# Kernel tuning notes

Measured on AMD Instinct MI355X. Metric: run time of the kernel, lower is better.

## Reference

```python
import jax, jax.numpy as jnp
import numpy as np

N_NODES = 100000
N_EDGES = 3200000
D_IN = 256
D_OUT = 256


def setup_inputs() -> dict:
    key = jax.random.key(0)
    k1, k2, k3, k4, k5 = jax.random.split(key, 5)
    x = jax.random.normal(k1, (N_NODES, D_IN), dtype=jnp.float32)
    weight = jax.random.normal(k2, (D_IN, D_OUT), dtype=jnp.float32)
    edge_rows = jax.random.randint(k3, (N_EDGES,), 0, N_NODES, dtype=jnp.int32)
    edge_cols = jax.random.randint(k4, (N_EDGES,), 0, N_NODES, dtype=jnp.int32)
    edge_vals = jax.random.uniform(k5, (N_EDGES,), dtype=jnp.float32)
    return {"x": x, "weight": weight, "edge_rows": edge_rows,
            "edge_cols": edge_cols, "edge_vals": edge_vals}


def reference(x, weight, edge_rows, edge_cols, edge_vals):
    # GraphConvolution forward (eval mode, dense features, no bias):
    #   xw  = x @ W                      [N, D_OUT]
    #   out = relu(A_sparse @ xw)        A given as COO edge list
    xw = x @ weight  # [N, D_OUT]
    msgs = edge_vals[:, None] * xw[edge_cols]  # gather source features, scale
    agg = jax.ops.segment_sum(msgs, edge_rows, num_segments=N_NODES)
    return jax.nn.relu(agg)
```

## Files before the change

kernel.cpp:

```cpp
#include <hip/hip_runtime.h>
#include <hip/hip_bf16.h>

#define N_NODES 100000
#define N_EDGES 3200000
#define D 256

#define RSH2 8
#define RPB2 256
#define NB2 ((N_NODES + RPB2 - 1) / RPB2)
#define FILL_CH 14336
#define NBLK_F ((N_EDGES + FILL_CH - 1) / FILL_CH)
#define MAX_BREC 9216

typedef __attribute__((ext_vector_type(8))) short short8;
typedef __attribute__((ext_vector_type(4))) float floatx4;

__device__ __forceinline__ unsigned short f32_to_bf16_rne(float f) {
    unsigned int u = __float_as_uint(f);
    u += 0x7FFFu + ((u >> 16) & 1u);
    return (unsigned short)(u >> 16);
}
__device__ __forceinline__ float bf16_bits_to_f32(unsigned short b) {
    return __uint_as_float(((unsigned int)b) << 16);
}
__device__ __forceinline__ float blo(unsigned int x) { return __uint_as_float(x << 16); }
__device__ __forceinline__ float bhi(unsigned int x) { return __uint_as_float(x & 0xFFFF0000u); }

__global__ __launch_bounds__(256) void convert_w_k(const float* __restrict__ w,
                                                   unsigned short* __restrict__ wsw) {
    int t = blockIdx.x * 256 + threadIdx.x;
    int j     = t & 7;
    int lane  = (t >> 3) & 63;
    int kstep = (t >> 9) & 7;
    int ntile = t >> 12;
    int k = kstep * 32 + (lane >> 4) * 8 + j;
    int n = ntile * 16 + (lane & 15);
    wsw[t] = f32_to_bf16_rne(w[k * D + n]);
}

__global__ __launch_bounds__(512) void gemm_xw_k(const float* __restrict__ x,
                                                 const unsigned short* __restrict__ wsw,
                                                 unsigned short* __restrict__ xwb) {
    __shared__ uint4 wlds[8192];
    const int tid = threadIdx.x;
#pragma unroll
    for (int i = 0; i < 16; ++i) {
        int idx = i * 512 + tid;
        wlds[idx] = ((const uint4*)wsw)[idx];
    }
    __syncthreads();

    const int lane = tid & 63;
    const int wave = tid >> 6;
    const int q    = lane >> 4;
    const int ml   = lane & 15;
    const long rowBase = (long)blockIdx.x * 128 + wave * 16;
    long arow = rowBase + ml;
    if (arow >= N_NODES) arow = 0;
    const float* xr = x + arow * (long)D;

    floatx4 acc[16];
#pragma unroll
    for (int i = 0; i < 16; ++i) acc[i] = (floatx4){0.f, 0.f, 0.f, 0.f};

    const short8* wfrag = (const short8*)wlds;

#pragma unroll
    for (int ks = 0; ks < 8; ++ks) {
        const float4 a0 = *(const float4*)(xr + ks * 32 + q * 8);
        const float4 a1 = *(const float4*)(xr + ks * 32 + q * 8 + 4);
        short8 af;
        af[0] = (short)f32_to_bf16_rne(a0.x);
        af[1] = (short)f32_to_bf16_rne(a0.y);
        af[2] = (short)f32_to_bf16_rne(a0.z);
        af[3] = (short)f32_to_bf16_rne(a0.w);
        af[4] = (short)f32_to_bf16_rne(a1.x);
        af[5] = (short)f32_to_bf16_rne(a1.y);
        af[6] = (short)f32_to_bf16_rne(a1.z);
        af[7] = (short)f32_to_bf16_rne(a1.w);
#pragma unroll
        for (int nt = 0; nt < 16; ++nt) {
            acc[nt] = __builtin_amdgcn_mfma_f32_16x16x32_bf16(
                af, wfrag[(nt * 8 + ks) * 64 + lane], acc[nt], 0, 0, 0);
        }
    }

#pragma unroll
    for (int nt = 0; nt < 16; ++nt) {
#pragma unroll
        for (int r = 0; r < 4; ++r) {
            long orow = rowBase + q * 4 + r;
            if (orow < N_NODES)
                xwb[orow * (long)D + nt * 16 + ml] = f32_to_bf16_rne(acc[nt][r]);
        }
    }
}

__global__ __launch_bounds__(256) void hist2_k(const int* __restrict__ erow,
                                               int* __restrict__ C) {
    __shared__ int h[NB2];
    const int tid = threadIdx.x;
    for (int i = tid; i < NB2; i += 256) h[i] = 0;
    __syncthreads();
    const int s = blockIdx.x * FILL_CH;
    const int e = min(s + FILL_CH, N_EDGES);
    for (int i = s + tid; i < e; i += 256) atomicAdd(&h[erow[i] >> RSH2], 1);
    __syncthreads();
    for (int b = tid; b < NB2; b += 256) C[b * NBLK_F + blockIdx.x] = h[b];
}

__global__ __launch_bounds__(256) void colprefix_k(int* __restrict__ C,
                                                   int* __restrict__ tot) {
    const int wave_id = blockIdx.x * 4 + (threadIdx.x >> 6);
    const int lane = threadIdx.x & 63;
    if (wave_id >= NB2) return;
    int* row = C + wave_id * NBLK_F;
    int run = 0;
#pragma unroll
    for (int ch = 0; ch < NBLK_F; ch += 64) {
        int idx = ch + lane;
        int v = (idx < NBLK_F) ? row[idx] : 0;
        int x = v;
#pragma unroll
        for (int d = 1; d < 64; d <<= 1) {
            int u = __shfl_up(x, d);
            if (lane >= d) x += u;
        }
        int excl = x - v;
        if (idx < NBLK_F) row[idx] = run + excl;
        run += __shfl(x, 63);
    }
    if (lane == 0) tot[wave_id] = run;
}

__global__ __launch_bounds__(512) void totscan_k(const int* __restrict__ tot,
                                                 int* __restrict__ bbase) {
    __shared__ int wsum[8];
    const int t = threadIdx.x;
    const int lane = t & 63;
    const int wv = t >> 6;
    int v = (t < NB2) ? tot[t] : 0;
    int x = v;
#pragma unroll
    for (int d = 1; d < 64; d <<= 1) {
        int u = __shfl_up(x, d);
        if (lane >= d) x += u;
    }
    if (lane == 63) wsum[wv] = x;
    __syncthreads();
    if (wv == 0) {
        int y = (lane < 8) ? wsum[lane] : 0;
#pragma unroll
        for (int d = 1; d < 8; d <<= 1) {
            int u = __shfl_up(y, d);
            if (lane >= d) y += u;
        }
        if (lane < 8) wsum[lane] = y;
    }
    __syncthreads();
    int excl = x - v + ((wv > 0) ? wsum[wv - 1] : 0);
    if (t < NB2) bbase[t] = excl;
    if (t == NB2 - 1) bbase[NB2] = excl + v;
}

__global__ __launch_bounds__(256) void binfill2_k(const int* __restrict__ erow,
                                                  const int* __restrict__ ecol,
                                                  const float* __restrict__ eval,
                                                  const int* __restrict__ C,
                                                  const int* __restrict__ bbase,
                                                  unsigned long long* __restrict__ recs) {
    __shared__ unsigned long long lrec[FILL_CH];
    __shared__ int h[NB2];
    __shared__ int cur[NB2];
    __shared__ int gb[NB2];
    __shared__ int wsum[4];
    const int tid = threadIdx.x;
    const int blk = blockIdx.x;
    const int s = blk * FILL_CH;
    const int e = min(s + FILL_CH, N_EDGES);

    for (int i = tid; i < NB2; i += 256) h[i] = 0;
    __syncthreads();

    for (int i = s + tid; i < e; i += 256) atomicAdd(&h[erow[i] >> RSH2], 1);
    __syncthreads();

    {
        const int b0 = 2 * tid, b1 = 2 * tid + 1;
        int v0 = (b0 < NB2) ? h[b0] : 0;
        int v1 = (b1 < NB2) ? h[b1] : 0;
        int sv = v0 + v1;
        const int lane = tid & 63;
        const int wv = tid >> 6;
        int x = sv;
#pragma unroll
        for (int d = 1; d < 64; d <<= 1) {
            int u = __shfl_up(x, d);
            if (lane >= d) x += u;
        }
        if (lane == 63) wsum[wv] = x;
        __syncthreads();
        if (wv == 0) {
            int y = (lane < 4) ? wsum[lane] : 0;
#pragma unroll
            for (int d = 1; d < 4; d <<= 1) {
                int u = __shfl_up(y, d);
                if (lane >= d) y += u;
            }
            if (lane < 4) wsum[lane] = y;
        }
        __syncthreads();
        int excl = x - sv + ((wv > 0) ? wsum[wv - 1] : 0);
        if (b0 < NB2) cur[b0] = excl;
        if (b1 < NB2) cur[b1] = excl + v0;
        for (int b = tid; b < NB2; b += 256) gb[b] = bbase[b] + C[b * NBLK_F + blk];
    }
    __syncthreads();

    for (int i = s + tid; i < e; i += 256) {
        int r = erow[i];
        int b = r >> RSH2;
        unsigned long long rec =
            ((unsigned long long)(r & (RPB2 - 1)) << 33) |
            ((unsigned long long)f32_to_bf16_rne(eval[i]) << 17) |
            (unsigned int)ecol[i];
        int pos = atomicAdd(&cur[b], 1);
        lrec[pos] = rec;
    }
    __syncthreads();

    const int lane = tid & 63;
    const int wv = tid >> 6;
    for (int b = wv; b < NB2; b += 4) {
        int len = h[b];
        int start = cur[b] - len;
        int gdst = gb[b];
        for (int o = lane; o < len; o += 64) recs[gdst + o] = lrec[start + o];
    }
}

__global__ __launch_bounds__(256) void bsort2_k(const int* __restrict__ bbase,
                                                const unsigned long long* __restrict__ recs,
                                                int* __restrict__ offsets,
                                                unsigned int* __restrict__ cs,
                                                unsigned short* __restrict__ vs) {
    __shared__ unsigned long long lrec[MAX_BREC];
    __shared__ int hist[RPB2];
    __shared__ int cur[RPB2];
    __shared__ int wsum[4];
    const int t = threadIdx.x;
    const int b = blockIdx.x;
    const int base = bbase[b];
    const int nfull = bbase[b + 1] - base;
    const int n = min(nfull, MAX_BREC);

    for (int i = t; i < n; i += 256) lrec[i] = recs[base + i];
    hist[t] = 0;
    __syncthreads();
    for (int i = t; i < nfull; i += 256) {
        unsigned long long rec = (i < n) ? lrec[i] : recs[base + i];
        atomicAdd(&hist[(int)((rec >> 33) & 255u)], 1);
    }
    __syncthreads();

    {
        int v = hist[t];
        const int lane = t & 63;
        const int wv = t >> 6;
        int x = v;
#pragma unroll
        for (int d = 1; d < 64; d <<= 1) {
            int u = __shfl_up(x, d);
            if (lane >= d) x += u;
        }
        if (lane == 63) wsum[wv] = x;
        __syncthreads();
        if (wv == 0) {
            int y = (lane < 4) ? wsum[lane] : 0;
#pragma unroll
            for (int d = 1; d < 4; d <<= 1) {
                int u = __shfl_up(y, d);
                if (lane >= d) y += u;
            }
            if (lane < 4) wsum[lane] = y;
        }
        __syncthreads();
        int excl = x - v + ((wv > 0) ? wsum[wv - 1] : 0);
        cur[t] = excl;
        int r = (b << RSH2) + t;
        if (r <= N_NODES) offsets[r] = base + excl;
    }
    __syncthreads();

    for (int i = t; i < nfull; i += 256) {
        unsigned long long rec = (i < n) ? lrec[i] : recs[base + i];
        int rl = (int)((rec >> 33) & 255u);
        int pos = base + atomicAdd(&cur[rl], 1);
        cs[pos] = (unsigned int)(rec & 0x1FFFFu);
        vs[pos] = (unsigned short)((rec >> 17) & 0xFFFFu);
    }
}

__global__ __launch_bounds__(256) void aggregate_k(const unsigned short* __restrict__ xwb,
                                                   const int* __restrict__ offsets,
                                                   const unsigned int* __restrict__ cs,
                                                   const unsigned short* __restrict__ vs,
                                                   float* __restrict__ out) {
    const int wave = threadIdx.x >> 6;
    const int lane = threadIdx.x & 63;
    const int r = blockIdx.x * 4 + wave;
    if (r >= N_NODES) return;

    const int start = offsets[r];
    const int end   = offsets[r + 1];
    const int half  = lane >> 5;
    const int hl    = lane & 31;

    float acc[8];
#pragma unroll
    for (int k = 0; k < 8; ++k) acc[k] = 0.f;

#pragma unroll 1
    for (int jb = start; jb < end; jb += 64) {
        int j = jb + lane;
        unsigned int c = 0;
        float v = 0.f;
        if (j < end) {
            c = cs[j];
            v = bf16_bits_to_f32(vs[j]);
        }
        const int cnt = min(64, end - jb);
        const int pairs = (cnt + 1) >> 1;
        const int hp = cnt >> 1;
        int t = 0;

#define FMA8(qv, bv)                                                           \
        acc[0] += bv * blo(qv.x); acc[1] += bv * bhi(qv.x);                    \
        acc[2] += bv * blo(qv.y); acc[3] += bv * bhi(qv.y);                    \
        acc[4] += bv * blo(qv.z); acc[5] += bv * bhi(qv.z);                    \
        acc[6] += bv * blo(qv.w); acc[7] += bv * bhi(qv.w);
#define SLOTF(s, qv, bv)                                                       \
        {                                                                      \
            int src = 2 * (t + (s)) + half;                                    \
            unsigned int bc = (unsigned int)__shfl((int)c, src);               \
            bv = __shfl(v, src);                                               \
            qv = ((const uint4*)(xwb + (size_t)bc * D))[hl];                   \
        }

#pragma unroll 1
        for (; t + 8 <= hp; t += 8) {
            uint4 q0, q1, q2, q3, q4, q5, q6, q7;
            float b0, b1, b2, b3, b4, b5, b6, b7;
            SLOTF(0, q0, b0) SLOTF(1, q1, b1) SLOTF(2, q2, b2) SLOTF(3, q3, b3)
            SLOTF(4, q4, b4) SLOTF(5, q5, b5) SLOTF(6, q6, b6) SLOTF(7, q7, b7)
            FMA8(q0, b0) FMA8(q1, b1) FMA8(q2, b2) FMA8(q3, b3)
            FMA8(q4, b4) FMA8(q5, b5) FMA8(q6, b6) FMA8(q7, b7)
        }
        if (t + 4 <= hp) {
            uint4 q0, q1, q2, q3;
            float b0, b1, b2, b3;
            SLOTF(0, q0, b0) SLOTF(1, q1, b1) SLOTF(2, q2, b2) SLOTF(3, q3, b3)
            FMA8(q0, b0) FMA8(q1, b1) FMA8(q2, b2) FMA8(q3, b3)
            t += 4;
        }
#undef SLOTF

#pragma unroll 1
        for (; t < pairs; ++t) {
            int src = 2 * t + half;
            int srcc = min(src, cnt - 1);
            unsigned int bc = (unsigned int)__shfl((int)c, srcc);
            float bb = __shfl(v, srcc);
            float bv = (src < cnt) ? bb : 0.f;
            uint4 q = ((const uint4*)(xwb + (size_t)bc * D))[hl];
            FMA8(q, bv)
        }
#undef FMA8
    }

#pragma unroll
    for (int k = 0; k < 8; ++k) acc[k] += __shfl_xor(acc[k], 32);

    const int s = lane >> 1;
    const int par = lane & 1;
    float4 o;
    {
        float a0 = __shfl(acc[0], s), b0 = __shfl(acc[4], s);
        float a1 = __shfl(acc[1], s), b1 = __shfl(acc[5], s);
        float a2 = __shfl(acc[2], s), b2 = __shfl(acc[6], s);
        float a3 = __shfl(acc[3], s), b3 = __shfl(acc[7], s);
        o.x = par ? b0 : a0;
        o.y = par ? b1 : a1;
        o.z = par ? b2 : a2;
        o.w = par ? b3 : a3;
    }
    o.x = fmaxf(o.x, 0.f);
    o.y = fmaxf(o.y, 0.f);
    o.z = fmaxf(o.z, 0.f);
    o.w = fmaxf(o.w, 0.f);
    ((float4*)(out + (size_t)r * D))[lane] = o;
}

extern "C" void kernel_launch(void* const* d_in, const int* in_sizes, int n_in,
                              void* d_out, int out_size, void* d_ws, size_t ws_size,
                              hipStream_t stream) {
    const float* x    = (const float*)d_in[0];
    const float* w    = (const float*)d_in[1];
    const int*   erow = (const int*)d_in[2];
    const int*   ecol = (const int*)d_in[3];
    const float* eval = (const float*)d_in[4];
    float* out = (float*)d_out;

    char* p = (char*)d_ws;
    auto align = [](size_t v) { return (v + 255) & ~(size_t)255; };

    unsigned short* xwb = (unsigned short*)p;
    p += align((size_t)N_NODES * D * sizeof(unsigned short));
    unsigned short* wsw = (unsigned short*)p;
    p += align((size_t)D * D * sizeof(unsigned short));
    int* C     = (int*)p;  p += align((size_t)NB2 * NBLK_F * sizeof(int));
    int* tot   = (int*)p;  p += align((size_t)NB2 * sizeof(int));
    int* bbase = (int*)p;  p += align((size_t)(NB2 + 1) * sizeof(int));
    unsigned long long* recs = (unsigned long long*)p;
    p += align((size_t)N_EDGES * sizeof(unsigned long long));
    unsigned int*   cs = (unsigned int*)p;    p += align((size_t)N_EDGES * 4);
    unsigned short* vs = (unsigned short*)p;  p += align((size_t)N_EDGES * 2);
    int* offsets = (int*)p;  p += align((size_t)(N_NODES + 1) * sizeof(int));

    convert_w_k<<<(D * D) / 256, 256, 0, stream>>>(w, wsw);
    gemm_xw_k<<<(N_NODES + 127) / 128, 512, 0, stream>>>(x, wsw, xwb);
    hist2_k<<<NBLK_F, 256, 0, stream>>>(erow, C);
    colprefix_k<<<(NB2 + 3) / 4, 256, 0, stream>>>(C, tot);
    totscan_k<<<1, 512, 0, stream>>>(tot, bbase);
    binfill2_k<<<NBLK_F, 256, 0, stream>>>(erow, ecol, eval, C, bbase, recs);
    bsort2_k<<<NB2, 256, 0, stream>>>(bbase, recs, offsets, cs, vs);
    aggregate_k<<<(N_NODES + 3) / 4, 256, 0, stream>>>(xwb, offsets, cs, vs, out);
}
```

Measured before the change: 564.8 us.

## Fuse per-bucket row sort into aggregation using 64-row buckets in LDS

```diff
diff --git a/kernel.cpp b/kernel.cpp
--- a/kernel.cpp
+++ b/kernel.cpp
@@ -5,12 +5,13 @@
 #define N_EDGES 3200000
 #define D 256
 
-#define RSH2 8
-#define RPB2 256
-#define NB2 ((N_NODES + RPB2 - 1) / RPB2)
+#define RSH3 6
+#define RPB3 64
+#define NB3 ((N_NODES + RPB3 - 1) / RPB3)
 #define FILL_CH 14336
 #define NBLK_F ((N_EDGES + FILL_CH - 1) / FILL_CH)
-#define MAX_BREC 9216
+#define BCAP 2560
+#define OCAP 64
 
 typedef __attribute__((ext_vector_type(8))) short short8;
 typedef __attribute__((ext_vector_type(4))) float floatx4;
@@ -98,22 +99,22 @@
 
 __global__ __launch_bounds__(256) void hist2_k(const int* __restrict__ erow,
                                                int* __restrict__ C) {
-    __shared__ int h[NB2];
+    __shared__ int h[NB3];
     const int tid = threadIdx.x;
-    for (int i = tid; i < NB2; i += 256) h[i] = 0;
+    for (int i = tid; i < NB3; i += 256) h[i] = 0;
     __syncthreads();
     const int s = blockIdx.x * FILL_CH;
     const int e = min(s + FILL_CH, N_EDGES);
-    for (int i = s + tid; i < e; i += 256) atomicAdd(&h[erow[i] >> RSH2], 1);
-    __syncthreads();
-    for (int b = tid; b < NB2; b += 256) C[b * NBLK_F + blockIdx.x] = h[b];
+    for (int i = s + tid; i < e; i += 256) atomicAdd(&h[erow[i] >> RSH3], 1);
+    __syncthreads();
+    for (int b = tid; b < NB3; b += 256) C[b * NBLK_F + blockIdx.x] = h[b];
 }
 
 __global__ __launch_bounds__(256) void colprefix_k(int* __restrict__ C,
                                                    int* __restrict__ tot) {
     const int wave_id = blockIdx.x * 4 + (threadIdx.x >> 6);
     const int lane = threadIdx.x & 63;
-    if (wave_id >= NB2) return;
+    if (wave_id >= NB3) return;
     int* row = C + wave_id * NBLK_F;
     int run = 0;
 #pragma unroll
@@ -133,14 +134,17 @@
     if (lane == 0) tot[wave_id] = run;
 }
 
-__global__ __launch_bounds__(512) void totscan_k(const int* __restrict__ tot,
-                                                 int* __restrict__ bbase) {
-    __shared__ int wsum[8];
+__global__ __launch_bounds__(1024) void totscan_k(const int* __restrict__ tot,
+                                                  int* __restrict__ bbase) {
+    __shared__ int wsum[16];
     const int t = threadIdx.x;
     const int lane = t & 63;
     const int wv = t >> 6;
-    int v = (t < NB2) ? tot[t] : 0;
-    int x = v;
+    const int b0 = 2 * t, b1 = 2 * t + 1;
+    int v0 = (b0 < NB3) ? tot[b0] : 0;
+    int v1 = (b1 < NB3) ? tot[b1] : 0;
+    int sv = v0 + v1;
+    int x = sv;
 #pragma unroll
     for (int d = 1; d < 64; d <<= 1) {
         int u = __shfl_up(x, d);
@@ -149,50 +153,54 @@
     if (lane == 63) wsum[wv] = x;
     __syncthreads();
     if (wv == 0) {
-        int y = (lane < 8) ? wsum[lane] : 0;
-#pragma unroll
-        for (int d = 1; d < 8; d <<= 1) {
+        int y = (lane < 16) ? wsum[lane] : 0;
+#pragma unroll
+        for (int d = 1; d < 16; d <<= 1) {
             int u = __shfl_up(y, d);
             if (lane >= d) y += u;
         }
-        if (lane < 8) wsum[lane] = y;
-    }
-    __syncthreads();
-    int excl = x - v + ((wv > 0) ? wsum[wv - 1] : 0);
-    if (t < NB2) bbase[t] = excl;
-    if (t == NB2 - 1) bbase[NB2] = excl + v;
-}
-
-__global__ __launch_bounds__(256) void binfill2_k(const int* __restrict__ erow,
+        if (lane < 16) wsum[lane] = y;
+    }
+    __syncthreads();
+    int excl = x - sv + ((wv > 0) ? wsum[wv - 1] : 0);
+    if (b0 < NB3) bbase[b0] = excl;
+    if (b1 < NB3) bbase[b1] = excl + v0;
+    if (b0 == NB3 - 1) bbase[NB3] = excl + v0;
+    if (b1 == NB3 - 1) bbase[NB3] = excl + v0 + v1;
+}
+
+__global__ __launch_bounds__(512) void binfill3_k(const int* __restrict__ erow,
                                                   const int* __restrict__ ecol,
                                                   const float* __restrict__ eval,
                                                   const int* __restrict__ C,
                                                   const int* __restrict__ bbase,
                                                   unsigned long long* __restrict__ recs) {
     __shared__ unsigned long long lrec[FILL_CH];
-    __shared__ int h[NB2];
-    __shared__ int cur[NB2];
-    __shared__ int gb[NB2];
-    __shared__ int wsum[4];
+    __shared__ int h[NB3];
+    __shared__ int cur[NB3];
+    __shared__ int gb[NB3];
+    __shared__ int wsum[8];
     const int tid = threadIdx.x;
     const int blk = blockIdx.x;
     const int s = blk * FILL_CH;
     const int e = min(s + FILL_CH, N_EDGES);
 
-    for (int i = tid; i < NB2; i += 256) h[i] = 0;
-    __syncthreads();
-
-    for (int i = s + tid; i < e; i += 256) atomicAdd(&h[erow[i] >> RSH2], 1);
+    for (int i = tid; i < NB3; i += 512) h[i] = 0;
+    __syncthreads();
+
+    for (int i = s + tid; i < e; i += 512) atomicAdd(&h[erow[i] >> RSH3], 1);
     __syncthreads();
 
     {
-        const int b0 = 2 * tid, b1 = 2 * tid + 1;
-        int v0 = (b0 < NB2) ? h[b0] : 0;
-        int v1 = (b1 < NB2) ? h[b1] : 0;
-        int sv = v0 + v1;
+        const int b0 = 4 * tid;
+        int v0 = (b0     < NB3) ? h[b0]     : 0;
+        int v1 = (b0 + 1 < NB3) ? h[b0 + 1] : 0;
+        int v2 = (b0 + 2 < NB3) ? h[b0 + 2] : 0;
+        int v3 = (b0 + 3 < NB3) ? h[b0 + 3] : 0;
+        int s4 = v0 + v1 + v2 + v3;
         const int lane = tid & 63;
         const int wv = tid >> 6;
-        int x = sv;
+        int x = s4;
 #pragma unroll
         for (int d = 1; d < 64; d <<= 1) {
             int u = __shfl_up(x, d);
@@ -201,27 +209,29 @@
         if (lane == 63) wsum[wv] = x;
         __syncthreads();
         if (wv == 0) {
-            int y = (lane < 4) ? wsum[lane] : 0;
-#pragma unroll
-            for (int d = 1; d < 4; d <<= 1) {
+            int y = (lane < 8) ? wsum[lane] : 0;
+#pragma unroll
+            for (int d = 1; d < 8; d <<= 1) {
                 int u = __shfl_up(y, d);
                 if (lane >= d) y += u;
             }
-            if (lane < 4) wsum[lane] = y;
+            if (lane < 8) wsum[lane] = y;
         }
         __syncthreads();
-        int excl = x - sv + ((wv > 0) ? wsum[wv - 1] : 0);
-        if (b0 < NB2) cur[b0] = excl;
-        if (b1 < NB2) cur[b1] = excl + v0;
-        for (int b = tid; b < NB2; b += 256) gb[b] = bbase[b] + C[b * NBLK_F + blk];
-    }
-    __syncthreads();
-
-    for (int i = s + tid; i < e; i += 256) {
+        int excl = x - s4 + ((wv > 0) ? wsum[wv - 1] : 0);
+        if (b0     < NB3) cur[b0]     = excl;
+        if (b0 + 1 < NB3) cur[b0 + 1] = excl + v0;
+        if (b0 + 2 < NB3) cur[b0 + 2] = excl + v0 + v1;
+        if (b0 + 3 < NB3) cur[b0 + 3] = excl + v0 + v1 + v2;
+    }
+    for (int b = tid; b < NB3; b += 512) gb[b] = bbase[b] + C[b * NBLK_F + blk];
+    __syncthreads();
+
+    for (int i = s + tid; i < e; i += 512) {
         int r = erow[i];
-        int b = r >> RSH2;
+        int b = r >> RSH3;
         unsigned long long rec =
-            ((unsigned long long)(r & (RPB2 - 1)) << 33) |
+            ((unsigned long long)(r & (RPB3 - 1)) << 33) |
             ((unsigned long long)f32_to_bf16_rne(eval[i]) << 17) |
             (unsigned int)ecol[i];
         int pos = atomicAdd(&cur[b], 1);
@@ -231,7 +241,7 @@
 
     const int lane = tid & 63;
     const int wv = tid >> 6;
-    for (int b = wv; b < NB2; b += 4) {
+    for (int b = wv; b < NB3; b += 8) {
         int len = h[b];
         int start = cur[b] - len;
         int gdst = gb[b];
@@ -239,166 +249,157 @@
     }
 }
 
-__global__ __launch_bounds__(256) void bsort2_k(const int* __restrict__ bbase,
-                                                const unsigned long long* __restrict__ recs,
-                                                int* __restrict__ offsets,
-                                                unsigned int* __restrict__ cs,
-                                                unsigned short* __restrict__ vs) {
-    __shared__ unsigned long long lrec[MAX_BREC];
-    __shared__ int hist[RPB2];
-    __shared__ int cur[RPB2];
-    __shared__ int wsum[4];
+__global__ __launch_bounds__(256) void baggr_k(const unsigned short* __restrict__ xwb,
+                                               const int* __restrict__ bbase,
+                                               const unsigned long long* __restrict__ recs,
+                                               float* __restrict__ out) {
+    __shared__ unsigned long long lrec[BCAP];
+    __shared__ unsigned long long ovfl[OCAP];
+    __shared__ int hist[RPB3];
+    __shared__ int cur[RPB3];
+    __shared__ int novf;
     const int t = threadIdx.x;
     const int b = blockIdx.x;
     const int base = bbase[b];
     const int nfull = bbase[b + 1] - base;
-    const int n = min(nfull, MAX_BREC);
-
-    for (int i = t; i < n; i += 256) lrec[i] = recs[base + i];
-    hist[t] = 0;
-    __syncthreads();
-    for (int i = t; i < nfull; i += 256) {
-        unsigned long long rec = (i < n) ? lrec[i] : recs[base + i];
-        atomicAdd(&hist[(int)((rec >> 33) & 255u)], 1);
-    }
-    __syncthreads();
-
-    {
+
+    if (t < RPB3) hist[t] = 0;
+    if (t == 0) novf = 0;
+    __syncthreads();
+    for (int i = t; i < nfull; i += 256)
+        atomicAdd(&hist[(int)((recs[base + i] >> 33) & 63u)], 1);
+    __syncthreads();
+
+    if (t < 64) {
         int v = hist[t];
-        const int lane = t & 63;
-        const int wv = t >> 6;
         int x = v;
 #pragma unroll
         for (int d = 1; d < 64; d <<= 1) {
             int u = __shfl_up(x, d);
-            if (lane >= d) x += u;
-        }
-        if (lane == 63) wsum[wv] = x;
-        __syncthreads();
-        if (wv == 0) {
-            int y = (lane < 4) ? wsum[lane] : 0;
-#pragma unroll
-            for (int d = 1; d < 4; d <<= 1) {
-                int u = __shfl_up(y, d);
-                if (lane >= d) y += u;
-            }
-            if (lane < 4) wsum[lane] = y;
-        }
-        __syncthreads();
-        int excl = x - v + ((wv > 0) ? wsum[wv - 1] : 0);
-        cur[t] = excl;
-        int r = (b << RSH2) + t;
-        if (r <= N_NODES) offsets[r] = base + excl;
+            if (t >= d) x += u;
+        }
+        cur[t] = x - v;
     }
     __syncthreads();
 
     for (int i = t; i < nfull; i += 256) {
-        unsigned long long rec = (i < n) ? lrec[i] : recs[base + i];
-        int rl = (int)((rec >> 33) & 255u);
-        int pos = base + atomicAdd(&cur[rl], 1);
-        cs[pos] = (unsigned int)(rec & 0x1FFFFu);
-        vs[pos] = (unsigned short)((rec >> 17) & 0xFFFFu);
-    }
-}
-
-__global__ __launch_bounds__(256) void aggregate_k(const unsigned short* __restrict__ xwb,
-                                                   const int* __restrict__ offsets,
-                                                   const unsigned int* __restrict__ cs,
-                                                   const unsigned short* __restrict__ vs,
-                                                   float* __restrict__ out) {
-    const int wave = threadIdx.x >> 6;
-    const int lane = threadIdx.x & 63;
-    const int r = blockIdx.x * 4 + wave;
-    if (r >= N_NODES) return;
-
-    const int start = offsets[r];
-    const int end   = offsets[r + 1];
-    const int half  = lane >> 5;
-    const int hl    = lane & 31;
-
-    float acc[8];
-#pragma unroll
-    for (int k = 0; k < 8; ++k) acc[k] = 0.f;
+        unsigned long long rec = recs[base + i];
+        int rl = (int)((rec >> 33) & 63u);
+        int pos = atomicAdd(&cur[rl], 1);
+        if (pos < BCAP) lrec[pos] = rec;
+        else {
+            int o = atomicAdd(&novf, 1);
+            if (o < OCAP) ovfl[o] = rec;
+        }
+    }
+    __syncthreads();
+
+    const int wave = t >> 6;
+    const int lane = t & 63;
+    const int half = lane >> 5;
+    const int hl   = lane & 31;
+    const int nov  = min(novf, OCAP);
 
 #pragma unroll 1
-    for (int jb = start; jb < end; jb += 64) {
-        int j = jb + lane;
-        unsigned int c = 0;
-        float v = 0.f;
-        if (j < end) {
-            c = cs[j];
-            v = bf16_bits_to_f32(vs[j]);
-        }
-        const int cnt = min(64, end - jb);
-        const int pairs = (cnt + 1) >> 1;
-        const int hp = cnt >> 1;
-        int t = 0;
+    for (int rr = 0; rr < 16; ++rr) {
+        const int rl = wave * 16 + rr;
+        const int r = (b << RSH3) + rl;
+        if (r >= N_NODES) break;
+        const int e_ = cur[rl];
+        const int s_ = e_ - hist[rl];
+        const int e = min(e_, BCAP);
+        const int s = min(s_, BCAP);
+
+        float acc[8];
+#pragma unroll
+        for (int k = 0; k < 8; ++k) acc[k] = 0.f;
+
+#pragma unroll 1
+        for (int jb = s; jb < e; jb += 64) {
+            const int cnt = min(64, e - jb);
+            const int pairs = (cnt + 1) >> 1;
+            const int hp = cnt >> 1;
+            int tt = 0;
 
 #define FMA8(qv, bv)                                                           \
-        acc[0] += bv * blo(qv.x); acc[1] += bv * bhi(qv.x);                    \
-        acc[2] += bv * blo(qv.y); acc[3] += bv * bhi(qv.y);                    \
-        acc[4] += bv * blo(qv.z); acc[5] += bv * bhi(qv.z);                    \
-        acc[6] += bv * blo(qv.w); acc[7] += bv * bhi(qv.w);
-#define SLOTF(s, qv, bv)                                                       \
-        {                                                                      \
-            int src = 2 * (t + (s)) + half;                                    \
-            unsigned int bc = (unsigned int)__shfl((int)c, src);               \
-            bv = __shfl(v, src);                                               \
-            qv = ((const uint4*)(xwb + (size_t)bc * D))[hl];                   \
-        }
+            acc[0] += bv * blo(qv.x); acc[1] += bv * bhi(qv.x);                \
+            acc[2] += bv * blo(qv.y); acc[3] += bv * bhi(qv.y);                \
+            acc[4] += bv * blo(qv.z); acc[5] += bv * bhi(qv.z);                \
+            acc[6] += bv * blo(qv.w); acc[7] += bv * bhi(qv.w);
+#define SLOTL(ss, qv, bv)                                                      \
+            {                                                                  \
+                int src = jb + 2 * (tt + (ss)) + half;                         \
+                unsigned long long rec = lrec[src];                            \
+                unsigned int bc = (unsigned int)(rec & 0x1FFFFu);              \
+                bv = bf16_bits_to_f32((unsigned short)((rec >> 17) & 0xFFFFu));\
+                qv = ((const uint4*)(xwb + (size_t)bc * D))[hl];               \
+            }
 
 #pragma unroll 1
-        for (; t + 8 <= hp; t += 8) {
-            uint4 q0, q1, q2, q3, q4, q5, q6, q7;
-            float b0, b1, b2, b3, b4, b5, b6, b7;
-            SLOTF(0, q0, b0) SLOTF(1, q1, b1) SLOTF(2, q2, b2) SLOTF(3, q3, b3)
-            SLOTF(4, q4, b4) SLOTF(5, q5, b5) SLOTF(6, q6, b6) SLOTF(7, q7, b7)
-            FMA8(q0, b0) FMA8(q1, b1) FMA8(q2, b2) FMA8(q3, b3)
-            FMA8(q4, b4) FMA8(q5, b5) FMA8(q6, b6) FMA8(q7, b7)
-        }
-        if (t + 4 <= hp) {
-            uint4 q0, q1, q2, q3;
-            float b0, b1, b2, b3;
-            SLOTF(0, q0, b0) SLOTF(1, q1, b1) SLOTF(2, q2, b2) SLOTF(3, q3, b3)
-            FMA8(q0, b0) FMA8(q1, b1) FMA8(q2, b2) FMA8(q3, b3)
-            t += 4;
-        }
-#undef SLOTF
-
+            for (; tt + 8 <= hp; tt += 8) {
+                uint4 q0, q1, q2, q3, q4, q5, q6, q7;
+                float b0, b1, b2, b3, b4, b5, b6, b7;
+                SLOTL(0, q0, b0) SLOTL(1, q1, b1) SLOTL(2, q2, b2) SLOTL(3, q3, b3)
+                SLOTL(4, q4, b4) SLOTL(5, q5, b5) SLOTL(6, q6, b6) SLOTL(7, q7, b7)
+                FMA8(q0, b0) FMA8(q1, b1) FMA8(q2, b2) FMA8(q3, b3)
+                FMA8(q4, b4) FMA8(q5, b5) FMA8(q6, b6) FMA8(q7, b7)
+            }
+            if (tt + 4 <= hp) {
+                uint4 q0, q1, q2, q3;
+                float b0, b1, b2, b3;
+                SLOTL(0, q0, b0) SLOTL(1, q1, b1) SLOTL(2, q2, b2) SLOTL(3, q3, b3)
+                FMA8(q0, b0) FMA8(q1, b1) FMA8(q2, b2) FMA8(q3, b3)
+                tt += 4;
+            }
+#undef SLOTL
 #pragma unroll 1
-        for (; t < pairs; ++t) {
-            int src = 2 * t + half;
-            int srcc = min(src, cnt - 1);
-            unsigned int bc = (unsigned int)__shfl((int)c, srcc);
-            float bb = __shfl(v, srcc);
-            float bv = (src < cnt) ? bb : 0.f;
-            uint4 q = ((const uint4*)(xwb + (size_t)bc * D))[hl];
-            FMA8(q, bv)
+            for (; tt < pairs; ++tt) {
+                int src = jb + 2 * tt + half;
+                int srcc = min(src, e - 1);
+                unsigned long long rec = lrec[srcc];
+                unsigned int bc = (unsigned int)(rec & 0x1FFFFu);
+                float vv = bf16_bits_to_f32((unsigned short)((rec >> 17) & 0xFFFFu));
+                float bv = (src < e) ? vv : 0.f;
+                uint4 q = ((const uint4*)(xwb + (size_t)bc * D))[hl];
+                FMA8(q, bv)
+            }
+        }
+
+#pragma unroll 1
+        for (int k = 0; k < nov; ++k) {
+            unsigned long long rec = ovfl[k];
+            if ((int)((rec >> 33) & 63u) == rl) {
+                unsigned int bc = (unsigned int)(rec & 0x1FFFFu);
+                float vv = bf16_bits_to_f32((unsigned short)((rec >> 17) & 0xFFFFu));
+                float bv = (half == 0) ? vv : 0.f;
+                uint4 q = ((const uint4*)(xwb + (size_t)bc * D))[hl];
+                FMA8(q, bv)
+            }
         }
 #undef FMA8
-    }
-
-#pragma unroll
-    for (int k = 0; k < 8; ++k) acc[k] += __shfl_xor(acc[k], 32);
-
-    const int s = lane >> 1;
-    const int par = lane & 1;
-    float4 o;
-    {
-        float a0 = __shfl(acc[0], s), b0 = __shfl(acc[4], s);
-        float a1 = __shfl(acc[1], s), b1 = __shfl(acc[5], s);
-        float a2 = __shfl(acc[2], s), b2 = __shfl(acc[6], s);
-        float a3 = __shfl(acc[3], s), b3 = __shfl(acc[7], s);
-        o.x = par ? b0 : a0;
-        o.y = par ? b1 : a1;
-        o.z = par ? b2 : a2;
-        o.w = par ? b3 : a3;
-    }
-    o.x = fmaxf(o.x, 0.f);
-    o.y = fmaxf(o.y, 0.f);
-    o.z = fmaxf(o.z, 0.f);
-    o.w = fmaxf(o.w, 0.f);
-    ((float4*)(out + (size_t)r * D))[lane] = o;
+
+#pragma unroll
+        for (int k = 0; k < 8; ++k) acc[k] += __shfl_xor(acc[k], 32);
+
+        const int sl = lane >> 1;
+        const int par = lane & 1;
+        float4 o;
+        {
+            float a0 = __shfl(acc[0], sl), c0 = __shfl(acc[4], sl);
+            float a1 = __shfl(acc[1], sl), c1 = __shfl(acc[5], sl);
+            float a2 = __shfl(acc[2], sl), c2 = __shfl(acc[6], sl);
+            float a3 = __shfl(acc[3], sl), c3 = __shfl(acc[7], sl);
+            o.x = par ? c0 : a0;
+            o.y = par ? c1 : a1;
+            o.z = par ? c2 : a2;
+            o.w = par ? c3 : a3;
+        }
+        o.x = fmaxf(o.x, 0.f);
+        o.y = fmaxf(o.y, 0.f);
+        o.z = fmaxf(o.z, 0.f);
+        o.w = fmaxf(o.w, 0.f);
+        ((float4*)(out + (size_t)r * D))[lane] = o;
+    }
 }
 
 extern "C" void kernel_launch(void* const* d_in, const int* in_sizes, int n_in,
@@ -418,21 +419,17 @@
     p += align((size_t)N_NODES * D * sizeof(unsigned short));
     unsigned short* wsw = (unsigned short*)p;
     p += align((size_t)D * D * sizeof(unsigned short));
-    int* C     = (int*)p;  p += align((size_t)NB2 * NBLK_F * sizeof(int));
-    int* tot   = (int*)p;  p += align((size_t)NB2 * sizeof(int));
-    int* bbase = (int*)p;  p += align((size_t)(NB2 + 1) * sizeof(int));
+    int* C     = (int*)p;  p += align((size_t)NB3 * NBLK_F * sizeof(int));
+    int* tot   = (int*)p;  p += align((size_t)NB3 * sizeof(int));
+    int* bbase = (int*)p;  p += align((size_t)(NB3 + 1) * sizeof(int));
     unsigned long long* recs = (unsigned long long*)p;
     p += align((size_t)N_EDGES * sizeof(unsigned long long));
-    unsigned int*   cs = (unsigned int*)p;    p += align((size_t)N_EDGES * 4);
-    unsigned short* vs = (unsigned short*)p;  p += align((size_t)N_EDGES * 2);
-    int* offsets = (int*)p;  p += align((size_t)(N_NODES + 1) * sizeof(int));
 
     convert_w_k<<<(D * D) / 256, 256, 0, stream>>>(w, wsw);
     gemm_xw_k<<<(N_NODES + 127) / 128, 512, 0, stream>>>(x, wsw, xwb);
     hist2_k<<<NBLK_F, 256, 0, stream>>>(erow, C);
-    colprefix_k<<<(NB2 + 3) / 4, 256, 0, stream>>>(C, tot);
-    totscan_k<<<1, 512, 0, stream>>>(tot, bbase);
-    binfill2_k<<<NBLK_F, 256, 0, stream>>>(erow, ecol, eval, C, bbase, recs);
-    bsort2_k<<<NB2, 256, 0, stream>>>(bbase, recs, offsets, cs, vs);
-    aggregate_k<<<(N_NODES + 3) / 4, 256, 0, stream>>>(xwb, offsets, cs, vs, out);
-}
+    colprefix_k<<<(NB3 + 3) / 4, 256, 0, stream>>>(C, tot);
+    totscan_k<<<1, 1024, 0, stream>>>(tot, bbase);
+    binfill3_k<<<NBLK_F, 512, 0, stream>>>(erow, ecol, eval, C, bbase, recs);
+    baggr_k<<<NB3, 256, 0, stream>>>(xwb, bbase, recs, out);
+}
```

After: 545.8 us. -3.4%, faster.
